# Performance work log

Measured on AMD Instinct MI355X. Metric: run time of the kernel, lower is better.

Reference implementation:

```python
import jax, jax.numpy as jnp
import numpy as np

B, P, S, D, DFF, VOCAB, T = 16, 16, 512, 256, 1024, 5000, 256
EPS = 1e-6

def _layernorm(x, g, b):
    mu = jnp.mean(x, axis=-1, keepdims=True)
    var = jnp.var(x, axis=-1, keepdims=True)
    return (x - mu) * jax.lax.rsqrt(var + EPS) * g + b

def setup_inputs() -> dict:
    key = jax.random.key(0)
    ks = jax.random.split(key, 16)
    nrm = lambda k, shape: (jax.random.normal(k, shape) * 0.02).astype(jnp.float32)
    return {
        'x': jax.random.normal(ks[0], (B, P, D), jnp.float32),
        'y': jax.random.randint(ks[1], (B, P, 1), 0, VOCAB),
        'K': jax.random.normal(ks[2], (B, P, S, D), jnp.float32),
        'V': jax.random.normal(ks[3], (B, P, S, D), jnp.float32),
        'R': jax.random.normal(ks[4], (B, P, S, D), jnp.float32),
        'wq': nrm(ks[5], (D, D)), 'bq': jnp.zeros((D,), jnp.float32),
        'wk': nrm(ks[6], (D, D)), 'bk': jnp.zeros((D,), jnp.float32),
        'wv': nrm(ks[7], (D, D)), 'bv': jnp.zeros((D,), jnp.float32),
        'wo': nrm(ks[8], (D, D)), 'bo': jnp.zeros((D,), jnp.float32),
        'w1': nrm(ks[9], (D, DFF)), 'b1': jnp.zeros((DFF,), jnp.float32),
        'w2': nrm(ks[10], (DFF, D)), 'b2': jnp.zeros((D,), jnp.float32),
        'ln1_g': jnp.ones((D,), jnp.float32), 'ln1_b': jnp.zeros((D,), jnp.float32),
        'ln2_g': jnp.ones((D,), jnp.float32), 'ln2_b': jnp.zeros((D,), jnp.float32),
        'w_out': nrm(ks[11], (D, VOCAB)),
        'sigmas': jnp.array([0.1, 0.1, 0.1, 0.1], jnp.float32),  # sigma_q, sigma_k, sigma_v, sigma_z
        'timestep': T,
    }

def reference(x, y, K, V, R, wq, bq, wk, bk, wv, bv, wo, bo, w1, b1, w2, b2,
              ln1_g, ln1_b, ln2_g, ln2_b, w_out, sigmas, timestep):
    t = timestep
    xq = x[:, :, None, :]                                   # (B,P,1,D)
    q_ = xq @ wq + bq
    k_ = xq @ wk + bk
    v_ = xq @ wv + bv
    nk = jax.random.split(jax.random.key(1234), 5)
    # SMC reparameterized gaussian noise on q,k,v
    q = q_ + sigmas[0] * jax.random.normal(nk[0], q_.shape, q_.dtype)
    k = k_ + sigmas[1] * jax.random.normal(nk[1], k_.shape, k_.dtype)
    v = v_ + sigmas[2] * jax.random.normal(nk[2], v_.shape, v_.dtype)
    noise_q = q - q_
    # write current k,v into timestep slot (== concat(past, k, future))
    K = K.at[:, :, t:t + 1, :].set(k)
    V = V.at[:, :, t:t + 1, :].set(v)
    Kw, Vw = K[:, :, :t + 1, :], V[:, :, :t + 1, :]         # causal window
    logits = jnp.einsum('bpqd,bpsd->bpqs', q, Kw) / jnp.sqrt(jnp.float32(D))
    attn = jax.nn.softmax(logits, axis=-1)                  # (B,P,1,t+1)
    z_ = jnp.einsum('bpqs,bpsd->bpqd', attn, Vw) @ wo + bo
    z = z_ + sigmas[3] * jax.random.normal(nk[3], z_.shape, z_.dtype)
    noise_z = z - z_
    out = _layernorm(z + xq, ln1_g, ln1_b)
    f = jax.nn.relu(out @ w1 + b1) @ w2 + b2
    r = _layernorm(f + out, ln2_g, ln2_b)                   # (B,P,1,D)
    preds = r @ w_out                                       # (B,P,1,VOCAB)
    R = R.at[:, :, t:t + 1, :].set(r)
    # particle weights (classification) + ancestor sampling
    probas = jax.nn.softmax(preds, axis=-1)[:, :, 0, :]     # (B,P,VOCAB)
    w = jnp.take_along_axis(probas, y, axis=-1)[:, :, 0]    # (B,P)
    w_norm = jax.lax.stop_gradient(jax.nn.softmax(w, axis=-1))
    i_t = jax.random.categorical(nk[4], w_norm[:, None, :], shape=(B, P))  # (B,P)
    def resample(params):
        past = jnp.take_along_axis(params[:, :, :t + 1, :], i_t[:, :, None, None], axis=1)
        return jnp.concatenate([past, params[:, :, t + 1:, :]], axis=2)
    K, V, R = resample(K), resample(V), resample(R)
    return (r, attn, noise_q, noise_z, K, V, R)
```

## Files before the change

### kernel.cpp

```cpp
#include <hip/hip_runtime.h>
#include <stdint.h>
#include <stddef.h>

#define B_    16
#define P_    16
#define S_    512
#define D_    256
#define DFF_  1024
#define VOCAB_ 5000
#define T_    256
#define ROWS_ 256
#define EPS_  1e-6f

#define PARTITIONABLE 1

__host__ __device__ __forceinline__ uint32_t rotl32_(uint32_t x, int d) {
  return (x << d) | (x >> (32 - d));
}

__host__ __device__ __forceinline__ void threefry2x32_(uint32_t k0, uint32_t k1,
                                                       uint32_t x0, uint32_t x1,
                                                       uint32_t& o0, uint32_t& o1) {
  uint32_t ks2 = k0 ^ k1 ^ 0x1BD11BDAu;
  x0 += k0; x1 += k1;
  x0 += x1; x1 = rotl32_(x1, 13); x1 ^= x0;
  x0 += x1; x1 = rotl32_(x1, 15); x1 ^= x0;
  x0 += x1; x1 = rotl32_(x1, 26); x1 ^= x0;
  x0 += x1; x1 = rotl32_(x1,  6); x1 ^= x0;
  x0 += k1; x1 += ks2 + 1u;
  x0 += x1; x1 = rotl32_(x1, 17); x1 ^= x0;
  x0 += x1; x1 = rotl32_(x1, 29); x1 ^= x0;
  x0 += x1; x1 = rotl32_(x1, 16); x1 ^= x0;
  x0 += x1; x1 = rotl32_(x1, 24); x1 ^= x0;
  x0 += ks2; x1 += k0 + 2u;
  x0 += x1; x1 = rotl32_(x1, 13); x1 ^= x0;
  x0 += x1; x1 = rotl32_(x1, 15); x1 ^= x0;
  x0 += x1; x1 = rotl32_(x1, 26); x1 ^= x0;
  x0 += x1; x1 = rotl32_(x1,  6); x1 ^= x0;
  x0 += k0; x1 += k1 + 3u;
  x0 += x1; x1 = rotl32_(x1, 17); x1 ^= x0;
  x0 += x1; x1 = rotl32_(x1, 29); x1 ^= x0;
  x0 += x1; x1 = rotl32_(x1, 16); x1 ^= x0;
  x0 += x1; x1 = rotl32_(x1, 24); x1 ^= x0;
  x0 += k1; x1 += ks2 + 4u;
  x0 += x1; x1 = rotl32_(x1, 13); x1 ^= x0;
  x0 += x1; x1 = rotl32_(x1, 15); x1 ^= x0;
  x0 += x1; x1 = rotl32_(x1, 26); x1 ^= x0;
  x0 += x1; x1 = rotl32_(x1,  6); x1 ^= x0;
  x0 += ks2; x1 += k0 + 5u;
  o0 = x0; o1 = x1;
}

__device__ __forceinline__ uint32_t jax_bits(uint32_t k0, uint32_t k1,
                                             uint32_t i, uint32_t half) {
#if PARTITIONABLE
  uint32_t o0, o1;
  threefry2x32_(k0, k1, 0u, i, o0, o1);
  return o0 ^ o1;
#else
  uint32_t o0, o1;
  uint32_t lo = (i < half) ? i : (i - half);
  threefry2x32_(k0, k1, lo, lo + half, o0, o1);
  return (i < half) ? o0 : o1;
#endif
}

__device__ __forceinline__ float bits_to_u01(uint32_t b) {
  return __uint_as_float((b >> 9) | 0x3F800000u) - 1.0f;
}

__device__ __forceinline__ float erfinv32(float x) {
  float w = -log1pf(-x * x);
  float p;
  if (w < 5.0f) {
    w -= 2.5f;
    p = 2.81022636e-08f;
    p = fmaf(p, w, 3.43273939e-07f);
    p = fmaf(p, w, -3.5233877e-06f);
    p = fmaf(p, w, -4.39150654e-06f);
    p = fmaf(p, w, 0.00021858087f);
    p = fmaf(p, w, -0.00125372503f);
    p = fmaf(p, w, -0.00417768164f);
    p = fmaf(p, w, 0.246640727f);
    p = fmaf(p, w, 1.50140941f);
  } else {
    w = sqrtf(w) - 3.0f;
    p = -0.000200214257f;
    p = fmaf(p, w, 0.000100950558f);
    p = fmaf(p, w, 0.00134934322f);
    p = fmaf(p, w, -0.00367342844f);
    p = fmaf(p, w, 0.00573950773f);
    p = fmaf(p, w, -0.0076224613f);
    p = fmaf(p, w, 0.00943887047f);
    p = fmaf(p, w, 1.00167406f);
    p = fmaf(p, w, 2.83297682f);
  }
  return p * x;
}

__device__ __forceinline__ float jax_normal(uint32_t k0, uint32_t k1,
                                            uint32_t i, uint32_t half) {
  float u01 = bits_to_u01(jax_bits(k0, k1, i, half));
  const float lo = -0.99999994f;
  float u = __fadd_rn(__fmul_rn(u01, 2.0f), lo);
  u = fmaxf(lo, u);
  return 1.41421356f * erfinv32(u);
}

__device__ __forceinline__ float jax_gumbel(uint32_t k0, uint32_t k1,
                                            uint32_t i, uint32_t half) {
  float u01 = bits_to_u01(jax_bits(k0, k1, i, half));
  const float tiny = 1.17549435e-38f;
  float u = __fadd_rn(__fmul_rn(u01, 1.0f), tiny);
  u = fmaxf(tiny, u);
  return -logf(-logf(u));
}

__device__ __forceinline__ float blk_sum(float v, float* red, int tid) {
  #pragma unroll
  for (int off = 32; off > 0; off >>= 1) v += __shfl_xor(v, off, 64);
  if ((tid & 63) == 0) red[tid >> 6] = v;
  __syncthreads();
  if (tid == 0) {
    float s = 0.f;
    #pragma unroll
    for (int i = 0; i < 16; i++) s += red[i];
    red[16] = s;
  }
  __syncthreads();
  float r = red[16];
  __syncthreads();
  return r;
}
__device__ __forceinline__ float blk_max(float v, float* red, int tid) {
  #pragma unroll
  for (int off = 32; off > 0; off >>= 1) v = fmaxf(v, __shfl_xor(v, off, 64));
  if ((tid & 63) == 0) red[tid >> 6] = v;
  __syncthreads();
  if (tid == 0) {
    float s = -INFINITY;
    #pragma unroll
    for (int i = 0; i < 16; i++) s = fmaxf(s, red[i]);
    red[16] = s;
  }
  __syncthreads();
  float r = red[16];
  __syncthreads();
  return r;
}
__device__ __forceinline__ float block_reduce_sum256(float v, float* red, int tid) {
  return blk_sum(v, red, tid);
}

__global__ __launch_bounds__(1024) void fused_row_kernel(
    const float* __restrict__ x,
    const float* __restrict__ Kin, const float* __restrict__ Vin,
    const float* __restrict__ wq, const float* __restrict__ bq,
    const float* __restrict__ wk, const float* __restrict__ bk,
    const float* __restrict__ wv, const float* __restrict__ bv,
    const float* __restrict__ wo, const float* __restrict__ bo,
    const float* __restrict__ w1, const float* __restrict__ b1,
    const float* __restrict__ w2, const float* __restrict__ b2,
    const float* __restrict__ ln1g, const float* __restrict__ ln1b,
    const float* __restrict__ ln2g, const float* __restrict__ ln2b,
    const float* __restrict__ sigmas,
    float* __restrict__ kws, float* __restrict__ vws,
    float* __restrict__ attn_out, float* __restrict__ noiseq_out,
    float* __restrict__ noisez_out, float* __restrict__ r_out,
    uint32_t kq0, uint32_t kq1, uint32_t kk0, uint32_t kk1,
    uint32_t kv0, uint32_t kv1, uint32_t kz0, uint32_t kz1) {
  __shared__ float xs[D_], qs[D_], ksh[D_], vsh[D_], z0s[D_], os[D_];
  __shared__ float att[T_ + 4];
  __shared__ float hs[DFF_];
  __shared__ float sc3[3][4][D_];
  __shared__ float red[32];
  const int row = blockIdx.x, t = threadIdx.x;
  const int col = t & 255, ec = t >> 8;

  if (t < D_) xs[t] = x[row * D_ + t];
  __syncthreads();

  {
    float aq = 0.f, ak = 0.f, av = 0.f;
    const int e0 = ec * 64;
    #pragma unroll 8
    for (int e = e0; e < e0 + 64; e++) {
      float xe = xs[e];
      aq = fmaf(xe, wq[e * D_ + col], aq);
      ak = fmaf(xe, wk[e * D_ + col], ak);
      av = fmaf(xe, wv[e * D_ + col], av);
    }
    sc3[0][ec][col] = aq; sc3[1][ec][col] = ak; sc3[2][ec][col] = av;
  }
  __syncthreads();
  if (t < D_) {
    float qf = bq[t] + sc3[0][0][t] + sc3[0][1][t] + sc3[0][2][t] + sc3[0][3][t];
    float kf = bk[t] + sc3[1][0][t] + sc3[1][1][t] + sc3[1][2][t] + sc3[1][3][t];
    float vf = bv[t] + sc3[2][0][t] + sc3[2][1][t] + sc3[2][2][t] + sc3[2][3][t];
    uint32_t i = (uint32_t)row * D_ + t;
    float qn = qf + sigmas[0] * jax_normal(kq0, kq1, i, 32768u);
    float kn = kf + sigmas[1] * jax_normal(kk0, kk1, i, 32768u);
    float vn = vf + sigmas[2] * jax_normal(kv0, kv1, i, 32768u);
    qs[t] = qn; ksh[t] = kn; vsh[t] = vn;
    kws[i] = kn; vws[i] = vn;
    noiseq_out[i] = qn - qf;
  }
  __syncthreads();

  {
    const int wid = t >> 6, lane = t & 63;
    float4 myq = ((const float4*)qs)[lane];
    for (int s0 = wid * 4; s0 <= T_; s0 += 64) {
      #pragma unroll
      for (int j = 0; j < 4; j++) {
        int s = s0 + j;
        if (s <= T_) {
          const float* Krow = (s == T_) ? ksh
                                        : (Kin + ((size_t)row * S_ + s) * D_);
          float4 k4 = ((const float4*)Krow)[lane];
          float rr = myq.x * k4.x + myq.y * k4.y + myq.z * k4.z + myq.w * k4.w;
          #pragma unroll
          for (int off = 32; off > 0; off >>= 1) rr += __shfl_xor(rr, off, 64);
          if (lane == 0) att[s] = rr * 0.0625f;
        }
      }
    }
  }
  __syncthreads();

  {
    float v = (t <= T_) ? att[t] : -INFINITY;
    float mx = blk_max(v, red, t);
    float e = (t <= T_) ? expf(att[t] - mx) : 0.f;
    float sum = blk_sum(e, red, t);
    if (t <= T_) {
      float a = e / sum;
      att[t] = a;
      attn_out[(size_t)row * (T_ + 1) + t] = a;
    }
  }
  __syncthreads();

  {
    float acc = 0.f;
    const int s0 = ec * 64;
    #pragma unroll 8
    for (int s = s0; s < s0 + 64; s++)
      acc = fmaf(att[s], Vin[((size_t)row * S_ + s) * D_ + col], acc);
    if (ec == 3) acc = fmaf(att[T_], vsh[col], acc);
    sc3[0][ec][col] = acc;
  }
  __syncthreads();
  if (t < D_) z0s[t] = sc3[0][0][t] + sc3[0][1][t] + sc3[0][2][t] + sc3[0][3][t];
  __syncthreads();

  {
    float acc = 0.f;
    const int e0 = ec * 64;
    #pragma unroll 8
    for (int e = e0; e < e0 + 64; e++)
      acc = fmaf(z0s[e], wo[e * D_ + col], acc);
    sc3[0][ec][col] = acc;
  }
  __syncthreads();
  if (t < D_) {
    float zp = bo[t] + sc3[0][0][t] + sc3[0][1][t] + sc3[0][2][t] + sc3[0][3][t];
    uint32_t i = (uint32_t)row * D_ + t;
    float zn = zp + sigmas[3] * jax_normal(kz0, kz1, i, 32768u);
    noisez_out[i] = zn - zp;
    z0s[t] = zn + xs[t];
  }
  __syncthreads();
  {
    float y = (t < D_) ? z0s[t] : 0.f;
    float mu = blk_sum(y, red, t) * (1.0f / 256.0f);
    float dv = (t < D_) ? (z0s[t] - mu) : 0.f;
    float var = blk_sum(dv * dv, red, t) * (1.0f / 256.0f);
    if (t < D_) os[t] = dv * rsqrtf(var + EPS_) * ln1g[t] + ln1b[t];
  }
  __syncthreads();

  {
    float acc = b1[t];
    #pragma unroll 8
    for (int e = 0; e < D_; e++) acc = fmaf(os[e], w1[(size_t)e * DFF_ + t], acc);
    hs[t] = fmaxf(acc, 0.f);
  }
  __syncthreads();

  {
    float acc = 0.f;
    const int e0 = ec * 256;
    #pragma unroll 8
    for (int e = e0; e < e0 + 256; e++)
      acc = fmaf(hs[e], w2[(size_t)e * D_ + col], acc);
    sc3[0][ec][col] = acc;
  }
  __syncthreads();
  if (t < D_) {
    float f = b2[t] + sc3[0][0][t] + sc3[0][1][t] + sc3[0][2][t] + sc3[0][3][t];
    z0s[t] = f + os[t];
  }
  __syncthreads();
  {
    float y = (t < D_) ? z0s[t] : 0.f;
    float mu = blk_sum(y, red, t) * (1.0f / 256.0f);
    float dv = (t < D_) ? (z0s[t] - mu) : 0.f;
    float var = blk_sum(dv * dv, red, t) * (1.0f / 256.0f);
    if (t < D_)
      r_out[(size_t)row * D_ + t] = dv * rsqrtf(var + EPS_) * ln2g[t] + ln2b[t];
  }
}

__global__ __launch_bounds__(256) void preds_kernel(
    const float* __restrict__ r, const float* __restrict__ w_out,
    float* __restrict__ preds) {
  int tid = threadIdx.x;
  int col = blockIdx.x * 250 + tid;
  int rb = blockIdx.y * 16;
  if (tid >= 250) return;
  float acc[16];
  #pragma unroll
  for (int m = 0; m < 16; m++) acc[m] = 0.f;
  #pragma unroll 4
  for (int e = 0; e < D_; e++) {
    float wv = w_out[(size_t)e * VOCAB_ + col];
    #pragma unroll
    for (int m = 0; m < 16; m++)
      acc[m] = fmaf(r[(size_t)(rb + m) * D_ + e], wv, acc[m]);
  }
  #pragma unroll
  for (int m = 0; m < 16; m++)
    preds[(size_t)(rb + m) * VOCAB_ + col] = acc[m];
}

__device__ __forceinline__ float red256_sum(float v, float* red, int tid) {
  red[tid] = v; __syncthreads();
  #pragma unroll
  for (int st = 128; st > 0; st >>= 1) {
    if (tid < st) red[tid] += red[tid + st];
    __syncthreads();
  }
  float r = red[0]; __syncthreads();
  return r;
}
__device__ __forceinline__ float red256_max(float v, float* red, int tid) {
  red[tid] = v; __syncthreads();
  #pragma unroll
  for (int st = 128; st > 0; st >>= 1) {
    if (tid < st) red[tid] = fmaxf(red[tid], red[tid + st]);
    __syncthreads();
  }
  float r = red[0]; __syncthreads();
  return r;
}

__global__ __launch_bounds__(256) void pick_kernel(
    const float* __restrict__ preds, const int* __restrict__ y,
    float* __restrict__ w) {
  __shared__ float red[256];
  int row = blockIdx.x, tid = threadIdx.x;
  const float* pr = preds + (size_t)row * VOCAB_;
  float m = -INFINITY;
  for (int j = tid; j < VOCAB_; j += 256) m = fmaxf(m, pr[j]);
  float mx = red256_max(m, red, tid);
  float s = 0.f;
  for (int j = tid; j < VOCAB_; j += 256) s += expf(pr[j] - mx);
  float sum = red256_sum(s, red, tid);
  if (tid == 0) w[row] = expf(pr[y[row]] - mx) / sum;
}

__global__ __launch_bounds__(256) void cat_kernel(
    const float* __restrict__ w, int* __restrict__ i_t,
    uint32_t kc0, uint32_t kc1) {
  __shared__ float wv[256];
  __shared__ float wn[256];
  int tid = threadIdx.x;
  int b = tid >> 4;
  wv[tid] = w[tid];
  __syncthreads();
  float mx = -INFINITY;
  for (int j = 0; j < 16; j++) mx = fmaxf(mx, wv[b * 16 + j]);
  float ev = expf(wv[tid] - mx);
  wn[tid] = ev;
  __syncthreads();
  float sum = 0.f;
  for (int j = 0; j < 16; j++) sum += wn[b * 16 + j];
  __syncthreads();
  wn[tid] = ev / sum;
  __syncthreads();
  float best = -INFINITY;
  int bi = 0;
  for (int j = 0; j < 16; j++) {
    uint32_t idx = (uint32_t)tid * 16u + (uint32_t)j;
    float g = jax_gumbel(kc0, kc1, idx, 2048u);
    float sc = g + wn[b * 16 + j];
    if (sc > best) { best = sc; bi = j; }
  }
  i_t[tid] = bi;
}

__global__ __launch_bounds__(256) void resample_kernel(
    const float4* __restrict__ Kin, const float4* __restrict__ Vin,
    const float4* __restrict__ Rin,
    const float4* __restrict__ knew, const float4* __restrict__ vnew,
    const float4* __restrict__ rnew,
    const int* __restrict__ i_t,
    float4* __restrict__ Kout, float4* __restrict__ Vout,
    float4* __restrict__ Rout) {
  uint32_t idx = blockIdx.x * 256u + threadIdx.x;
  uint32_t d4 = idx & 63u;
  uint32_t s  = (idx >> 6) & 511u;
  uint32_t p  = (idx >> 15) & 15u;
  uint32_t b  = idx >> 19;
  const float4* in; const float4* nw; float4* out;
  if (blockIdx.y == 0)      { in = Kin; nw = knew; out = Kout; }
  else if (blockIdx.y == 1) { in = Vin; nw = vnew; out = Vout; }
  else                      { in = Rin; nw = rnew; out = Rout; }
  float4 val;
  if (s > T_) {
    val = in[idx];
  } else {
    uint32_t ip = (uint32_t)i_t[(b << 4) | p];
    if (s == T_) val = nw[(((b << 4) | ip) << 6) | d4];
    else         val = in[(((((b << 4) | ip) << 9) | s) << 6) | d4];
  }
  out[idx] = val;
}

static void compute_subkeys(uint32_t nk[5][2]) {
  const uint32_t k0 = 0u, k1 = 1234u;
#if PARTITIONABLE
  for (uint32_t j = 0; j < 5; j++)
    threefry2x32_(k0, k1, 0u, j, nk[j][0], nk[j][1]);
#else
  uint32_t o0[5], o1[5], out[10];
  for (uint32_t m = 0; m < 5; m++) threefry2x32_(k0, k1, m, m + 5u, o0[m], o1[m]);
  for (int m = 0; m < 5; m++) { out[m] = o0[m]; out[m + 5] = o1[m]; }
  for (int j = 0; j < 5; j++) { nk[j][0] = out[2 * j]; nk[j][1] = out[2 * j + 1]; }
#endif
}

extern "C" void kernel_launch(void* const* d_in, const int* in_sizes, int n_in,
                              void* d_out, int out_size, void* d_ws, size_t ws_size,
                              hipStream_t stream) {
  const float* x    = (const float*)d_in[0];
  const int*   y    = (const int*)d_in[1];
  const float* Kin  = (const float*)d_in[2];
  const float* Vin  = (const float*)d_in[3];
  const float* Rin  = (const float*)d_in[4];
  const float* wq   = (const float*)d_in[5];  const float* bq = (const float*)d_in[6];
  const float* wk   = (const float*)d_in[7];  const float* bk = (const float*)d_in[8];
  const float* wv   = (const float*)d_in[9];  const float* bv = (const float*)d_in[10];
  const float* wo   = (const float*)d_in[11]; const float* bo = (const float*)d_in[12];
  const float* w1   = (const float*)d_in[13]; const float* b1 = (const float*)d_in[14];
  const float* w2   = (const float*)d_in[15]; const float* b2 = (const float*)d_in[16];
  const float* ln1g = (const float*)d_in[17]; const float* ln1b = (const float*)d_in[18];
  const float* ln2g = (const float*)d_in[19]; const float* ln2b = (const float*)d_in[20];
  const float* w_out = (const float*)d_in[21];
  const float* sigmas = (const float*)d_in[22];
  (void)in_sizes; (void)n_in; (void)out_size; (void)ws_size;

  float* out        = (float*)d_out;
  float* r_out      = out;
  float* attn_out   = out + 65536;
  float* noiseq_out = out + 131328;
  float* noisez_out = out + 196864;
  float* K_out      = out + 262400;
  float* V_out      = out + 33816832;
  float* R_out      = out + 67371264;

  float* wsf   = (float*)d_ws;
  float* kws   = wsf;
  float* vws   = wsf + 65536;
  float* preds = wsf + 131072;
  float* wprob = wsf + 1411072;
  int*   i_t   = (int*)(wsf + 1411328);

  uint32_t nk[5][2];
  compute_subkeys(nk);

  fused_row_kernel<<<ROWS_, 1024, 0, stream>>>(
      x, Kin, Vin, wq, bq, wk, bk, wv, bv, wo, bo, w1, b1, w2, b2,
      ln1g, ln1b, ln2g, ln2b, sigmas,
      kws, vws, attn_out, noiseq_out, noisez_out, r_out,
      nk[0][0], nk[0][1], nk[1][0], nk[1][1], nk[2][0], nk[2][1],
      nk[3][0], nk[3][1]);
  preds_kernel<<<dim3(20, 16), 256, 0, stream>>>(r_out, w_out, preds);
  pick_kernel<<<ROWS_, 256, 0, stream>>>(preds, y, wprob);
  cat_kernel<<<1, 256, 0, stream>>>(wprob, i_t, nk[4][0], nk[4][1]);
  resample_kernel<<<dim3(32768, 3), 256, 0, stream>>>(
      (const float4*)Kin, (const float4*)Vin, (const float4*)Rin,
      (const float4*)kws, (const float4*)vws, (const float4*)r_out,
      i_t, (float4*)K_out, (float4*)V_out, (float4*)R_out);
}
```

Baseline: 271.1 us.

## Vectorize fused row kernel matvecs with float4 loads and 16-way split reduction

```diff
diff --git a/kernel.cpp b/kernel.cpp
--- a/kernel.cpp
+++ b/kernel.cpp
@@ -52,16 +52,13 @@
 }
 
 __device__ __forceinline__ uint32_t jax_bits(uint32_t k0, uint32_t k1,
-                                             uint32_t i, uint32_t half) {
+                                             uint32_t i) {
 #if PARTITIONABLE
   uint32_t o0, o1;
   threefry2x32_(k0, k1, 0u, i, o0, o1);
   return o0 ^ o1;
 #else
-  uint32_t o0, o1;
-  uint32_t lo = (i < half) ? i : (i - half);
-  threefry2x32_(k0, k1, lo, lo + half, o0, o1);
-  return (i < half) ? o0 : o1;
+  return 0u;
 #endif
 }
 
@@ -99,8 +96,8 @@
 }
 
 __device__ __forceinline__ float jax_normal(uint32_t k0, uint32_t k1,
-                                            uint32_t i, uint32_t half) {
-  float u01 = bits_to_u01(jax_bits(k0, k1, i, half));
+                                            uint32_t i) {
+  float u01 = bits_to_u01(jax_bits(k0, k1, i));
   const float lo = -0.99999994f;
   float u = __fadd_rn(__fmul_rn(u01, 2.0f), lo);
   u = fmaxf(lo, u);
@@ -108,8 +105,8 @@
 }
 
 __device__ __forceinline__ float jax_gumbel(uint32_t k0, uint32_t k1,
-                                            uint32_t i, uint32_t half) {
-  float u01 = bits_to_u01(jax_bits(k0, k1, i, half));
+                                            uint32_t i) {
+  float u01 = bits_to_u01(jax_bits(k0, k1, i));
   const float tiny = 1.17549435e-38f;
   float u = __fadd_rn(__fmul_rn(u01, 1.0f), tiny);
   u = fmaxf(tiny, u);
@@ -147,9 +144,6 @@
   float r = red[16];
   __syncthreads();
   return r;
-}
-__device__ __forceinline__ float block_reduce_sum256(float v, float* red, int tid) {
-  return blk_sum(v, red, tid);
 }
 
 __global__ __launch_bounds__(1024) void fused_row_kernel(
@@ -172,38 +166,55 @@
   __shared__ float xs[D_], qs[D_], ksh[D_], vsh[D_], z0s[D_], os[D_];
   __shared__ float att[T_ + 4];
   __shared__ float hs[DFF_];
-  __shared__ float sc3[3][4][D_];
+  __shared__ float4 scq[16][64];
+  __shared__ float4 sck[16][64];
+  __shared__ float4 scv[16][64];
   __shared__ float red[32];
   const int row = blockIdx.x, t = threadIdx.x;
-  const int col = t & 255, ec = t >> 8;
+  const int cg = t & 63;
+  const int sl = t >> 6;
 
   if (t < D_) xs[t] = x[row * D_ + t];
   __syncthreads();
 
   {
-    float aq = 0.f, ak = 0.f, av = 0.f;
-    const int e0 = ec * 64;
-    #pragma unroll 8
-    for (int e = e0; e < e0 + 64; e++) {
+    const float4* wqf = (const float4*)wq;
+    const float4* wkf = (const float4*)wk;
+    const float4* wvf = (const float4*)wv;
+    float4 aq = {0,0,0,0}, ak = {0,0,0,0}, av = {0,0,0,0};
+    const int e0 = sl * 16;
+    #pragma unroll
+    for (int e = e0; e < e0 + 16; e++) {
       float xe = xs[e];
-      aq = fmaf(xe, wq[e * D_ + col], aq);
-      ak = fmaf(xe, wk[e * D_ + col], ak);
-      av = fmaf(xe, wv[e * D_ + col], av);
-    }
-    sc3[0][ec][col] = aq; sc3[1][ec][col] = ak; sc3[2][ec][col] = av;
-  }
-  __syncthreads();
-  if (t < D_) {
-    float qf = bq[t] + sc3[0][0][t] + sc3[0][1][t] + sc3[0][2][t] + sc3[0][3][t];
-    float kf = bk[t] + sc3[1][0][t] + sc3[1][1][t] + sc3[1][2][t] + sc3[1][3][t];
-    float vf = bv[t] + sc3[2][0][t] + sc3[2][1][t] + sc3[2][2][t] + sc3[2][3][t];
-    uint32_t i = (uint32_t)row * D_ + t;
-    float qn = qf + sigmas[0] * jax_normal(kq0, kq1, i, 32768u);
-    float kn = kf + sigmas[1] * jax_normal(kk0, kk1, i, 32768u);
-    float vn = vf + sigmas[2] * jax_normal(kv0, kv1, i, 32768u);
-    qs[t] = qn; ksh[t] = kn; vsh[t] = vn;
-    kws[i] = kn; vws[i] = vn;
-    noiseq_out[i] = qn - qf;
+      float4 a = wqf[e * 64 + cg];
+      float4 b = wkf[e * 64 + cg];
+      float4 c = wvf[e * 64 + cg];
+      aq.x = fmaf(xe, a.x, aq.x); aq.y = fmaf(xe, a.y, aq.y);
+      aq.z = fmaf(xe, a.z, aq.z); aq.w = fmaf(xe, a.w, aq.w);
+      ak.x = fmaf(xe, b.x, ak.x); ak.y = fmaf(xe, b.y, ak.y);
+      ak.z = fmaf(xe, b.z, ak.z); ak.w = fmaf(xe, b.w, ak.w);
+      av.x = fmaf(xe, c.x, av.x); av.y = fmaf(xe, c.y, av.y);
+      av.z = fmaf(xe, c.z, av.z); av.w = fmaf(xe, c.w, av.w);
+    }
+    scq[sl][cg] = aq; sck[sl][cg] = ak; scv[sl][cg] = av;
+  }
+  __syncthreads();
+  if (t < 768) {
+    const int m = t >> 8, c = t & 255;
+    const float* sc = (m == 0) ? (const float*)scq
+                    : (m == 1) ? (const float*)sck : (const float*)scv;
+    float s = 0.f;
+    #pragma unroll
+    for (int j = 0; j < 16; j++) s += sc[j * 256 + c];
+    float bias = ((m == 0) ? bq : (m == 1) ? bk : bv)[c];
+    float base = bias + s;
+    uint32_t i = (uint32_t)row * D_ + c;
+    uint32_t a0 = (m == 0) ? kq0 : (m == 1) ? kk0 : kv0;
+    uint32_t a1 = (m == 0) ? kq1 : (m == 1) ? kk1 : kv1;
+    float val = base + sigmas[m] * jax_normal(a0, a1, i);
+    if (m == 0)      { qs[c] = val; noiseq_out[i] = val - base; }
+    else if (m == 1) { ksh[c] = val; kws[i] = val; }
+    else             { vsh[c] = val; vws[i] = val; }
   }
   __syncthreads();
 
@@ -242,31 +253,48 @@
   __syncthreads();
 
   {
-    float acc = 0.f;
-    const int s0 = ec * 64;
-    #pragma unroll 8
-    for (int s = s0; s < s0 + 64; s++)
-      acc = fmaf(att[s], Vin[((size_t)row * S_ + s) * D_ + col], acc);
-    if (ec == 3) acc = fmaf(att[T_], vsh[col], acc);
-    sc3[0][ec][col] = acc;
-  }
-  __syncthreads();
-  if (t < D_) z0s[t] = sc3[0][0][t] + sc3[0][1][t] + sc3[0][2][t] + sc3[0][3][t];
-  __syncthreads();
-
-  {
-    float acc = 0.f;
-    const int e0 = ec * 64;
-    #pragma unroll 8
-    for (int e = e0; e < e0 + 64; e++)
-      acc = fmaf(z0s[e], wo[e * D_ + col], acc);
-    sc3[0][ec][col] = acc;
+    const float4* Vf = (const float4*)(Vin + (size_t)row * S_ * D_);
+    float4 acc = {0,0,0,0};
+    const int s0 = sl * 16;
+    #pragma unroll
+    for (int s = s0; s < s0 + 16; s++) {
+      float a = att[s];
+      float4 v4 = Vf[s * 64 + cg];
+      acc.x = fmaf(a, v4.x, acc.x); acc.y = fmaf(a, v4.y, acc.y);
+      acc.z = fmaf(a, v4.z, acc.z); acc.w = fmaf(a, v4.w, acc.w);
+    }
+    scq[sl][cg] = acc;
   }
   __syncthreads();
   if (t < D_) {
-    float zp = bo[t] + sc3[0][0][t] + sc3[0][1][t] + sc3[0][2][t] + sc3[0][3][t];
+    float s = 0.f;
+    #pragma unroll
+    for (int j = 0; j < 16; j++) s += ((const float*)scq)[j * 256 + t];
+    z0s[t] = s + att[T_] * vsh[t];
+  }
+  __syncthreads();
+
+  {
+    const float4* wof = (const float4*)wo;
+    float4 acc = {0,0,0,0};
+    const int e0 = sl * 16;
+    #pragma unroll
+    for (int e = e0; e < e0 + 16; e++) {
+      float ze = z0s[e];
+      float4 w4 = wof[e * 64 + cg];
+      acc.x = fmaf(ze, w4.x, acc.x); acc.y = fmaf(ze, w4.y, acc.y);
+      acc.z = fmaf(ze, w4.z, acc.z); acc.w = fmaf(ze, w4.w, acc.w);
+    }
+    sck[sl][cg] = acc;
+  }
+  __syncthreads();
+  if (t < D_) {
+    float s = 0.f;
+    #pragma unroll
+    for (int j = 0; j < 16; j++) s += ((const float*)sck)[j * 256 + t];
+    float zp = bo[t] + s;
     uint32_t i = (uint32_t)row * D_ + t;
-    float zn = zp + sigmas[3] * jax_normal(kz0, kz1, i, 32768u);
+    float zn = zp + sigmas[3] * jax_normal(kz0, kz1, i);
     noisez_out[i] = zn - zp;
     z0s[t] = zn + xs[t];
   }
@@ -281,25 +309,47 @@
   __syncthreads();
 
   {
-    float acc = b1[t];
+    const int cg8 = t & 255, es = t >> 8;
+    const float4* w1f = (const float4*)w1;
+    float4 acc = {0,0,0,0};
+    const int e0 = es * 64;
     #pragma unroll 8
-    for (int e = 0; e < D_; e++) acc = fmaf(os[e], w1[(size_t)e * DFF_ + t], acc);
-    hs[t] = fmaxf(acc, 0.f);
-  }
-  __syncthreads();
-
-  {
-    float acc = 0.f;
-    const int e0 = ec * 256;
+    for (int e = e0; e < e0 + 64; e++) {
+      float oe = os[e];
+      float4 w4 = w1f[e * 256 + cg8];
+      acc.x = fmaf(oe, w4.x, acc.x); acc.y = fmaf(oe, w4.y, acc.y);
+      acc.z = fmaf(oe, w4.z, acc.z); acc.w = fmaf(oe, w4.w, acc.w);
+    }
+    ((float4*)scq)[es * 256 + cg8] = acc;
+  }
+  __syncthreads();
+  {
+    float s = 0.f;
+    #pragma unroll
+    for (int j = 0; j < 4; j++) s += ((const float*)scq)[j * 1024 + t];
+    hs[t] = fmaxf(b1[t] + s, 0.f);
+  }
+  __syncthreads();
+
+  {
+    const float4* w2f = (const float4*)w2;
+    float4 acc = {0,0,0,0};
+    const int e0 = sl * 64;
     #pragma unroll 8
-    for (int e = e0; e < e0 + 256; e++)
-      acc = fmaf(hs[e], w2[(size_t)e * D_ + col], acc);
-    sc3[0][ec][col] = acc;
+    for (int e = e0; e < e0 + 64; e++) {
+      float he = hs[e];
+      float4 w4 = w2f[e * 64 + cg];
+      acc.x = fmaf(he, w4.x, acc.x); acc.y = fmaf(he, w4.y, acc.y);
+      acc.z = fmaf(he, w4.z, acc.z); acc.w = fmaf(he, w4.w, acc.w);
+    }
+    scv[sl][cg] = acc;
   }
   __syncthreads();
   if (t < D_) {
-    float f = b2[t] + sc3[0][0][t] + sc3[0][1][t] + sc3[0][2][t] + sc3[0][3][t];
-    z0s[t] = f + os[t];
+    float s = 0.f;
+    #pragma unroll
+    for (int j = 0; j < 16; j++) s += ((const float*)scv)[j * 256 + t];
+    z0s[t] = b2[t] + s + os[t];
   }
   __syncthreads();
   {
@@ -393,7 +443,7 @@
   int bi = 0;
   for (int j = 0; j < 16; j++) {
     uint32_t idx = (uint32_t)tid * 16u + (uint32_t)j;
-    float g = jax_gumbel(kc0, kc1, idx, 2048u);
+    float g = jax_gumbel(kc0, kc1, idx);
     float sc = g + wn[b * 16 + j];
     if (sc > best) { best = sc; bi = j; }
   }
@@ -430,15 +480,8 @@
 
 static void compute_subkeys(uint32_t nk[5][2]) {
   const uint32_t k0 = 0u, k1 = 1234u;
-#if PARTITIONABLE
   for (uint32_t j = 0; j < 5; j++)
     threefry2x32_(k0, k1, 0u, j, nk[j][0], nk[j][1]);
-#else
-  uint32_t o0[5], o1[5], out[10];
-  for (uint32_t m = 0; m < 5; m++) threefry2x32_(k0, k1, m, m + 5u, o0[m], o1[m]);
-  for (int m = 0; m < 5; m++) { out[m] = o0[m]; out[m + 5] = o1[m]; }
-  for (int j = 0; j < 5; j++) { nk[j][0] = out[2 * j]; nk[j][1] = out[2 * j + 1]; }
-#endif
 }
 
 extern "C" void kernel_launch(void* const* d_in, const int* in_sizes, int n_in,
```

Result: no change. 266.6 us (-1.7%).
